# Performance work log

Hardware: AMD Instinct MI355X
Metric: run time of the kernel (lower is better)

Reference implementation:

```python
import jax, jax.numpy as jnp
import numpy as np

CDTYPE = jnp.complex64

# ---- 2x2 gate matrices (batched over events when theta is a vector) ----

def _rx(theta):
    h = theta * 0.5
    c = jnp.cos(h).astype(CDTYPE)
    s = (-1j) * jnp.sin(h).astype(CDTYPE)
    return jnp.stack([jnp.stack([c, s], -1), jnp.stack([s, c], -1)], -2)

def _ry(theta):
    h = theta * 0.5
    c = jnp.cos(h).astype(CDTYPE)
    s = jnp.sin(h).astype(CDTYPE)
    return jnp.stack([jnp.stack([c, -s], -1), jnp.stack([s, c], -1)], -2)

def _rz(theta):
    h = theta.astype(CDTYPE) * 0.5
    e0 = jnp.exp(-1j * h)
    e1 = jnp.exp(1j * h)
    z = jnp.zeros_like(e0)
    return jnp.stack([jnp.stack([e0, z], -1), jnp.stack([z, e1], -1)], -2)

# ---- batched statevector primitives (PennyLane convention: wire 0 = MSB) ----

def _apply(state, gate, wire):
    # state: (B, 2**n) complex; gate: (B,2,2) batched or (2,2) shared
    B = state.shape[0]
    st = state.reshape(B, 2 ** wire, 2, -1)
    if gate.ndim == 3:
        out = jnp.einsum('bij,bajc->baic', gate, st)
    else:
        out = jnp.einsum('ij,bajc->baic', gate, st)
    return out.reshape(B, -1)

def _cnot(state, c, t, n):
    # flip target axis on the control=1 half (pure permutation)
    B = state.shape[0]
    s = state.reshape((B,) + (2,) * n)
    i0 = [slice(None)] * (n + 1); i0[c + 1] = slice(0, 1)
    i1 = [slice(None)] * (n + 1); i1[c + 1] = slice(1, 2)
    s1 = jnp.flip(s[tuple(i1)], axis=t + 1)
    return jnp.concatenate([s[tuple(i0)], s1], axis=c + 1).reshape(B, -1)

def _expz(state, w):
    B = state.shape[0]
    p = (state.real ** 2 + state.imag ** 2).reshape(B, 2 ** w, 2, -1)
    return jnp.sum(p[:, :, 0, :], axis=(1, 2)) - jnp.sum(p[:, :, 1, :], axis=(1, 2))

def _qae_block(pt, eta, phi, weights, n, latent, trash, depth):
    B = pt.shape[0]
    state = jnp.zeros((B, 2 ** n), CDTYPE).at[:, 0].set(1.0)
    # angle encoding: RX(eta) RY(pt) RZ(phi) per wire (RX(0)=I covers MET)
    for k in range(n):
        state = _apply(state, _rx(eta[:, k]), k)
        state = _apply(state, _ry(pt[:, k]), k)
        state = _apply(state, _rz(phi[:, k]), k)
    for d in range(depth):
        for t in trash:
            for l in latent:
                state = _cnot(state, t, l, n)
        for k in range(n):
            state = _apply(state, _ry(weights[d * n + k]), k)  # shared (2,2) gate
        for l in latent:
            for t in trash:
                state = _cnot(state, l, t, n)
    return jnp.stack([_expz(state, w) for w in trash], axis=1)

def _forward(x, met_w, ele_w, mu_w, jet_w):
    B = x.shape[0]
    z = jnp.zeros((B, 1), x.dtype)
    met = _qae_block(x[:, 0:1], z, x[:, 1:2], met_w, 1, [], [0], 1)
    ele = _qae_block(x[:, 2:6], x[:, 6:10], x[:, 10:14], ele_w, 4, [0, 1], [2, 3], 1)
    mu = _qae_block(x[:, 14:18], x[:, 18:22], x[:, 22:26], mu_w, 4, [0, 1], [2, 3], 1)
    jet = _qae_block(x[:, 26:36], x[:, 36:46], x[:, 46:56], jet_w, 10,
                     [0, 1, 2, 3, 4, 5], [6, 7, 8, 9], 4)
    return met, ele, mu, jet

def setup_inputs() -> dict:
    key = jax.random.key(0)
    k0, k1, k2, k3, k4 = jax.random.split(key, 5)
    B = 4096
    return {
        'x': jax.random.normal(k0, (B, 56), dtype=jnp.float32),
        'met_weights': 0.01 * jax.random.normal(k1, (1,), dtype=jnp.float32),
        'ele_weights': 0.01 * jax.random.normal(k2, (4,), dtype=jnp.float32),
        'mu_weights': 0.01 * jax.random.normal(k3, (4,), dtype=jnp.float32),
        'jet_weights': 0.01 * jax.random.normal(k4, (40,), dtype=jnp.float32),
    }

def reference(x, met_weights, ele_weights, mu_weights, jet_weights):
    # returns (met (B,1), ele (B,2), mu (B,2), jet (B,4)) trash-wire Z expectations
    return _forward(x, met_weights, ele_weights, mu_weights, jet_weights)
```

## Files before the change

### kernel.cpp

```cpp
#include <hip/hip_runtime.h>
#include <hip/hip_bf16.h>


struct cplx { float re, im; };

__device__ __forceinline__ cplx cmul(cplx a, cplx b) {
  cplx r; r.re = a.re*b.re - a.im*b.im; r.im = a.re*b.im + a.im*b.re; return r;
}
__device__ __forceinline__ cplx csel(int c, cplx a, cplx b) {
  cplx r; r.re = c ? a.re : b.re; r.im = c ? a.im : b.im; return r;
}
__device__ __forceinline__ cplx shflx(cplx v, int m) {
  cplx r; r.re = __shfl_xor(v.re, m, 64); r.im = __shfl_xor(v.im, m, 64); return r;
}

__device__ __forceinline__ void enc_col(float pt, float eta, float phi,
                                        cplx* A, cplx* Bq) {
  float cx = __cosf(0.5f*eta), sx = __sinf(0.5f*eta);
  float cy = __cosf(0.5f*pt),  sy = __sinf(0.5f*pt);
  float cz = __cosf(0.5f*phi), sz = __sinf(0.5f*phi);
  float u = cy*cx, v = sy*sx;
  float p = sy*cx, q = -cy*sx;
  A->re  = cz*u + sz*v;  A->im  = cz*v - sz*u;
  Bq->re = cz*p - sz*q;  Bq->im = cz*q + sz*p;
}

__device__ void jet_sim(const float* __restrict__ xr, const float* __restrict__ jw,
                        float* __restrict__ out, int b, int lane, int jet_off) {
  cplx A[10], Bw[10];
  #pragma unroll
  for (int k = 0; k < 10; ++k)
    enc_col(xr[26+k], xr[36+k], xr[46+k], &A[k], &Bw[k]);

  cplx lf = csel((lane >> 5) & 1, Bw[4], A[4]);
  #pragma unroll
  for (int k = 5; k < 10; ++k)
    lf = cmul(lf, csel((lane >> (9-k)) & 1, Bw[k], A[k]));

  cplx st[16];
  #pragma unroll
  for (int r = 0; r < 16; ++r) {
    cplx f = lf;
    #pragma unroll
    for (int k = 0; k < 4; ++k)
      f = cmul(f, csel((r >> (3-k)) & 1, Bw[k], A[k]));
    st[r] = f;
  }

  const int p1 = __popc(lane & 15) & 1;
  const int lp = __popc(lane >> 4) & 1;

  for (int d = 0; d < 4; ++d) {
    #pragma unroll
    for (int r = 0; r < 8; ++r) {
      cplx v1 = st[r], v2 = st[r^15];
      cplx o1 = shflx(v2, 48);
      cplx o2 = shflx(v1, 48);
      st[r]    = csel(p1, o1, v1);
      st[r^15] = csel(p1, o2, v2);
    }
    float c[10], s[10];
    #pragma unroll
    for (int k = 0; k < 10; ++k) {
      float a = 0.5f * jw[d*10 + k];
      c[k] = __cosf(a); s[k] = __sinf(a);
    }
    #pragma unroll
    for (int k = 0; k < 4; ++k) {
      const int mr = 1 << (3-k);
      #pragma unroll
      for (int r = 0; r < 16; ++r) {
        if (!(r & mr)) {
          cplx a = st[r], bb = st[r|mr];
          st[r].re    = c[k]*a.re - s[k]*bb.re;
          st[r].im    = c[k]*a.im - s[k]*bb.im;
          st[r|mr].re = s[k]*a.re + c[k]*bb.re;
          st[r|mr].im = s[k]*a.im + c[k]*bb.im;
        }
      }
    }
    #pragma unroll
    for (int k = 4; k < 10; ++k) {
      const int lm = 1 << (9-k);
      const float sg = (lane & lm) ? s[k] : -s[k];
      #pragma unroll
      for (int r = 0; r < 16; ++r) {
        cplx o = shflx(st[r], lm);
        st[r].re = c[k]*st[r].re + sg*o.re;
        st[r].im = c[k]*st[r].im + sg*o.im;
      }
    }
    #pragma unroll
    for (int r = 0; r < 16; ++r) {
      cplx o = shflx(st[r], 15);
      const int p2 = (lp ^ (__popc(r) & 1)) & 1;
      st[r] = csel(p2, o, st[r]);
    }
  }

  float pr = 0.f;
  #pragma unroll
  for (int r = 0; r < 16; ++r)
    pr += st[r].re*st[r].re + st[r].im*st[r].im;
  pr += __shfl_xor(pr, 16, 64);
  pr += __shfl_xor(pr, 32, 64);
  float y = pr;
  #pragma unroll
  for (int j = 1; j <= 8; j <<= 1) {
    float aa = __shfl_xor(y, j, 64);
    y = (lane & j) ? (aa - y) : (y + aa);
  }
  if (lane == 8) out[jet_off + b*4 + 0] = y;
  if (lane == 4) out[jet_off + b*4 + 1] = y;
  if (lane == 2) out[jet_off + b*4 + 2] = y;
  if (lane == 1) out[jet_off + b*4 + 3] = y;
}

__device__ void sim4(const float* __restrict__ pt, const float* __restrict__ eta,
                     const float* __restrict__ phi, const float* __restrict__ w,
                     float* z_w2, float* z_w3) {
  cplx A[4], Bw[4];
  #pragma unroll
  for (int k = 0; k < 4; ++k)
    enc_col(pt[k], eta[k], phi[k], &A[k], &Bw[k]);

  cplx st[16];
  #pragma unroll
  for (int i = 0; i < 16; ++i) {
    cplx f = csel((i>>3)&1, Bw[0], A[0]);
    f = cmul(f, csel((i>>2)&1, Bw[1], A[1]));
    f = cmul(f, csel((i>>1)&1, Bw[2], A[2]));
    f = cmul(f, csel( i    &1, Bw[3], A[3]));
    st[i] = f;
  }
  cplx t;
  t = st[1]; st[1] = st[13]; st[13] = t;
  t = st[2]; st[2] = st[14]; st[14] = t;
  t = st[5]; st[5] = st[9];  st[9]  = t;
  t = st[6]; st[6] = st[10]; st[10] = t;
  #pragma unroll
  for (int k = 0; k < 4; ++k) {
    float a5 = 0.5f * w[k];
    float c = __cosf(a5), s = __sinf(a5);
    const int m = 8 >> k;
    #pragma unroll
    for (int i = 0; i < 16; ++i) {
      if (!(i & m)) {
        cplx a = st[i], bb = st[i|m];
        st[i].re   = c*a.re - s*bb.re;  st[i].im   = c*a.im - s*bb.im;
        st[i|m].re = s*a.re + c*bb.re;  st[i|m].im = s*a.im + c*bb.im;
      }
    }
  }
  t = st[4]; st[4] = st[7];  st[7]  = t;
  t = st[5]; st[5] = st[6];  st[6]  = t;
  t = st[8]; st[8] = st[11]; st[11] = t;
  t = st[9]; st[9] = st[10]; st[10] = t;

  float z2 = 0.f, z3 = 0.f;
  #pragma unroll
  for (int i = 0; i < 16; ++i) {
    float p = st[i].re*st[i].re + st[i].im*st[i].im;
    z2 += ((i>>1)&1) ? -p : p;
    z3 += ( i    &1) ? -p : p;
  }
  *z_w2 = z2; *z_w3 = z3;
}

__global__ __launch_bounds__(256)
void qae_kernel(const float* __restrict__ x,
                const float* __restrict__ met_w,
                const float* __restrict__ ele_w,
                const float* __restrict__ mu_w,
                const float* __restrict__ jet_w,
                float* __restrict__ out, int B, int jet_blocks) {
  if ((int)blockIdx.x < jet_blocks) {
    int wave = blockIdx.x * 4 + (threadIdx.x >> 6);
    int lane = threadIdx.x & 63;
    if (wave < B)
      jet_sim(x + (size_t)wave*56, jet_w, out, wave, lane, 5*B);
  } else {
    int b = (blockIdx.x - jet_blocks) * 256 + threadIdx.x;
    if (b >= B) return;
    const float* xr = x + (size_t)b*56;
    {
      float pt = xr[0], phi = xr[1], mw = met_w[0];
      float cy = __cosf(0.5f*pt),  sy = __sinf(0.5f*pt);
      float cz = __cosf(0.5f*phi), sz = __sinf(0.5f*phi);
      float cw = __cosf(0.5f*mw),  sw = __sinf(0.5f*mw);
      cplx al; al.re = cz*cy; al.im = -sz*cy;
      cplx be; be.re = cz*sy; be.im =  sz*sy;
      cplx a0; a0.re = cw*al.re - sw*be.re; a0.im = cw*al.im - sw*be.im;
      cplx a1; a1.re = sw*al.re + cw*be.re; a1.im = sw*al.im + cw*be.im;
      out[b] = (a0.re*a0.re + a0.im*a0.im) - (a1.re*a1.re + a1.im*a1.im);
    }
    float z2, z3;
    sim4(xr+2,  xr+6,  xr+10, ele_w, &z2, &z3);
    out[B   + b*2 + 0] = z2;  out[B   + b*2 + 1] = z3;
    sim4(xr+14, xr+18, xr+22, mu_w, &z2, &z3);
    out[3*B + b*2 + 0] = z2;  out[3*B + b*2 + 1] = z3;
  }
}

extern "C" void kernel_launch(void* const* d_in, const int* in_sizes, int n_in,
                              void* d_out, int out_size, void* d_ws, size_t ws_size,
                              hipStream_t stream) {
  const float* x     = (const float*)d_in[0];
  const float* met_w = (const float*)d_in[1];
  const float* ele_w = (const float*)d_in[2];
  const float* mu_w  = (const float*)d_in[3];
  const float* jet_w = (const float*)d_in[4];
  float* out = (float*)d_out;
  int B = in_sizes[0] / 56;
  int jet_blocks   = (B * 64 + 255) / 256;
  int small_blocks = (B + 255) / 256;
  qae_kernel<<<dim3(jet_blocks + small_blocks), dim3(256), 0, stream>>>(
      x, met_w, ele_w, mu_w, jet_w, out, B, jet_blocks);
}
```

Measured before the change: 106.0 us.

## Split each jet event's statevector across two waves with LDS exchange

Each jet event now runs on a 128-thread block, two waves, instead of one wave. Each lane holds 8 amplitudes instead of 16, and one qubit (wire 6) is mapped to the wave index. That qubit's gate and CNOT mixing are done through a shared-memory exchange with the partner wave, using block barriers. The aim is to halve per-thread register state and raise parallelism and occupancy, at the cost of LDS traffic, __syncthreads per depth layer, and a final cross-wave reduction.

```diff
diff --git a/kernel.cpp b/kernel.cpp
--- a/kernel.cpp
+++ b/kernel.cpp
@@ -25,97 +25,6 @@
   Bq->re = cz*p - sz*q;  Bq->im = cz*q + sz*p;
 }
 
-__device__ void jet_sim(const float* __restrict__ xr, const float* __restrict__ jw,
-                        float* __restrict__ out, int b, int lane, int jet_off) {
-  cplx A[10], Bw[10];
-  #pragma unroll
-  for (int k = 0; k < 10; ++k)
-    enc_col(xr[26+k], xr[36+k], xr[46+k], &A[k], &Bw[k]);
-
-  cplx lf = csel((lane >> 5) & 1, Bw[4], A[4]);
-  #pragma unroll
-  for (int k = 5; k < 10; ++k)
-    lf = cmul(lf, csel((lane >> (9-k)) & 1, Bw[k], A[k]));
-
-  cplx st[16];
-  #pragma unroll
-  for (int r = 0; r < 16; ++r) {
-    cplx f = lf;
-    #pragma unroll
-    for (int k = 0; k < 4; ++k)
-      f = cmul(f, csel((r >> (3-k)) & 1, Bw[k], A[k]));
-    st[r] = f;
-  }
-
-  const int p1 = __popc(lane & 15) & 1;
-  const int lp = __popc(lane >> 4) & 1;
-
-  for (int d = 0; d < 4; ++d) {
-    #pragma unroll
-    for (int r = 0; r < 8; ++r) {
-      cplx v1 = st[r], v2 = st[r^15];
-      cplx o1 = shflx(v2, 48);
-      cplx o2 = shflx(v1, 48);
-      st[r]    = csel(p1, o1, v1);
-      st[r^15] = csel(p1, o2, v2);
-    }
-    float c[10], s[10];
-    #pragma unroll
-    for (int k = 0; k < 10; ++k) {
-      float a = 0.5f * jw[d*10 + k];
-      c[k] = __cosf(a); s[k] = __sinf(a);
-    }
-    #pragma unroll
-    for (int k = 0; k < 4; ++k) {
-      const int mr = 1 << (3-k);
-      #pragma unroll
-      for (int r = 0; r < 16; ++r) {
-        if (!(r & mr)) {
-          cplx a = st[r], bb = st[r|mr];
-          st[r].re    = c[k]*a.re - s[k]*bb.re;
-          st[r].im    = c[k]*a.im - s[k]*bb.im;
-          st[r|mr].re = s[k]*a.re + c[k]*bb.re;
-          st[r|mr].im = s[k]*a.im + c[k]*bb.im;
-        }
-      }
-    }
-    #pragma unroll
-    for (int k = 4; k < 10; ++k) {
-      const int lm = 1 << (9-k);
-      const float sg = (lane & lm) ? s[k] : -s[k];
-      #pragma unroll
-      for (int r = 0; r < 16; ++r) {
-        cplx o = shflx(st[r], lm);
-        st[r].re = c[k]*st[r].re + sg*o.re;
-        st[r].im = c[k]*st[r].im + sg*o.im;
-      }
-    }
-    #pragma unroll
-    for (int r = 0; r < 16; ++r) {
-      cplx o = shflx(st[r], 15);
-      const int p2 = (lp ^ (__popc(r) & 1)) & 1;
-      st[r] = csel(p2, o, st[r]);
-    }
-  }
-
-  float pr = 0.f;
-  #pragma unroll
-  for (int r = 0; r < 16; ++r)
-    pr += st[r].re*st[r].re + st[r].im*st[r].im;
-  pr += __shfl_xor(pr, 16, 64);
-  pr += __shfl_xor(pr, 32, 64);
-  float y = pr;
-  #pragma unroll
-  for (int j = 1; j <= 8; j <<= 1) {
-    float aa = __shfl_xor(y, j, 64);
-    y = (lane & j) ? (aa - y) : (y + aa);
-  }
-  if (lane == 8) out[jet_off + b*4 + 0] = y;
-  if (lane == 4) out[jet_off + b*4 + 1] = y;
-  if (lane == 2) out[jet_off + b*4 + 2] = y;
-  if (lane == 1) out[jet_off + b*4 + 3] = y;
-}
-
 __device__ void sim4(const float* __restrict__ pt, const float* __restrict__ eta,
                      const float* __restrict__ phi, const float* __restrict__ w,
                      float* z_w2, float* z_w3) {
@@ -167,20 +76,135 @@
   *z_w2 = z2; *z_w3 = z3;
 }
 
-__global__ __launch_bounds__(256)
+__global__ __launch_bounds__(128)
 void qae_kernel(const float* __restrict__ x,
                 const float* __restrict__ met_w,
                 const float* __restrict__ ele_w,
                 const float* __restrict__ mu_w,
                 const float* __restrict__ jet_w,
-                float* __restrict__ out, int B, int jet_blocks) {
-  if ((int)blockIdx.x < jet_blocks) {
-    int wave = blockIdx.x * 4 + (threadIdx.x >> 6);
-    int lane = threadIdx.x & 63;
-    if (wave < B)
-      jet_sim(x + (size_t)wave*56, jet_w, out, wave, lane, 5*B);
+                float* __restrict__ out, int B) {
+  __shared__ float sm[128*18 + 16];
+  if ((int)blockIdx.x < B) {
+    const int b    = blockIdx.x;
+    const int tid  = threadIdx.x;
+    const int lane = tid & 63;
+    const int w    = tid >> 6;
+    const float* xr = x + (size_t)b*56;
+
+    cplx A[10], Bw[10];
+    #pragma unroll
+    for (int k = 0; k < 10; ++k)
+      enc_col(xr[26+k], xr[36+k], xr[46+k], &A[k], &Bw[k]);
+
+    cplx lf = csel((lane>>5)&1, Bw[3], A[3]);
+    lf = cmul(lf, csel((lane>>4)&1, Bw[4], A[4]));
+    lf = cmul(lf, csel((lane>>3)&1, Bw[5], A[5]));
+    lf = cmul(lf, csel(w,           Bw[6], A[6]));
+    lf = cmul(lf, csel((lane>>2)&1, Bw[7], A[7]));
+    lf = cmul(lf, csel((lane>>1)&1, Bw[8], A[8]));
+    lf = cmul(lf, csel( lane    &1, Bw[9], A[9]));
+
+    cplx st[8];
+    #pragma unroll
+    for (int r = 0; r < 8; ++r) {
+      cplx f = cmul(lf, csel((r>>2)&1, Bw[0], A[0]));
+      f = cmul(f, csel((r>>1)&1, Bw[1], A[1]));
+      f = cmul(f, csel( r    &1, Bw[2], A[2]));
+      st[r] = f;
+    }
+
+    const int pt_par  = (__popc(lane & 7) + w) & 1;
+    const int pl_lane = __popc((lane>>3) & 7) & 1;
+    float2* myb = (float2*)(sm + tid*18);
+    float2* pb  = (float2*)(sm + (tid^64)*18);
+
+    #pragma unroll
+    for (int d = 0; d < 4; ++d) {
+      #pragma unroll
+      for (int r = 0; r < 4; ++r) {
+        cplx v1 = st[r], v2 = st[r^7];
+        cplx o1 = shflx(v2, 0x38), o2 = shflx(v1, 0x38);
+        st[r]   = csel(pt_par, o1, v1);
+        st[r^7] = csel(pt_par, o2, v2);
+      }
+      float c[10], s[10];
+      #pragma unroll
+      for (int k = 0; k < 10; ++k) {
+        float a = 0.5f * jet_w[d*10 + k];
+        c[k] = __cosf(a); s[k] = __sinf(a);
+      }
+      #pragma unroll
+      for (int k = 0; k < 3; ++k) {
+        const int mr = 4 >> k;
+        #pragma unroll
+        for (int r = 0; r < 8; ++r) {
+          if (!(r & mr)) {
+            cplx a = st[r], bb = st[r|mr];
+            st[r].re    = c[k]*a.re - s[k]*bb.re;
+            st[r].im    = c[k]*a.im - s[k]*bb.im;
+            st[r|mr].re = s[k]*a.re + c[k]*bb.re;
+            st[r|mr].im = s[k]*a.im + c[k]*bb.im;
+          }
+        }
+      }
+      #pragma unroll
+      for (int kk = 0; kk < 6; ++kk) {
+        const int k  = (kk < 3) ? (3 + kk) : (4 + kk);
+        const int lm = (kk < 3) ? (32 >> kk) : (4 >> (kk-3));
+        const float sg = (lane & lm) ? s[k] : -s[k];
+        #pragma unroll
+        for (int r = 0; r < 8; ++r) {
+          cplx o = shflx(st[r], lm);
+          st[r].re = c[k]*st[r].re + sg*o.re;
+          st[r].im = c[k]*st[r].im + sg*o.im;
+        }
+      }
+      #pragma unroll
+      for (int r = 0; r < 8; ++r) myb[r] = make_float2(st[r].re, st[r].im);
+      __syncthreads();
+      cplx q[8];
+      #pragma unroll
+      for (int r = 0; r < 8; ++r) { float2 v = pb[r]; q[r].re = v.x; q[r].im = v.y; }
+      __syncthreads();
+      const float sg6 = w ? s[6] : -s[6];
+      #pragma unroll
+      for (int r = 0; r < 8; ++r) {
+        cplx keep;
+        keep.re = c[6]*st[r].re + sg6*q[r].re;
+        keep.im = c[6]*st[r].im + sg6*q[r].im;
+        cplx qs = shflx(q[r], 7), ss = shflx(st[r], 7);
+        cplx mov;
+        mov.re = c[6]*qs.re - sg6*ss.re;
+        mov.im = c[6]*qs.im - sg6*ss.im;
+        const int pl = (pl_lane + __popc(r)) & 1;
+        st[r] = csel(pl, mov, keep);
+      }
+    }
+
+    float pr = 0.f;
+    #pragma unroll
+    for (int r = 0; r < 8; ++r) pr += st[r].re*st[r].re + st[r].im*st[r].im;
+    pr += __shfl_xor(pr, 8, 64);
+    pr += __shfl_xor(pr, 16, 64);
+    pr += __shfl_xor(pr, 32, 64);
+    float y = pr;
+    #pragma unroll
+    for (int j = 1; j <= 4; j <<= 1) {
+      float aa = __shfl_xor(y, j, 64);
+      y = (lane & j) ? (aa - y) : (y + aa);
+    }
+    float* red = sm + 128*18;
+    if (lane < 8) red[w*8 + lane] = y;
+    __syncthreads();
+    if (tid == 0) {
+      float* o = out + (size_t)5*B + (size_t)b*4;
+      o[0] = red[0] - red[8];
+      o[1] = red[4] + red[12];
+      o[2] = red[2] + red[10];
+      o[3] = red[1] + red[9];
+    }
   } else {
-    int b = (blockIdx.x - jet_blocks) * 256 + threadIdx.x;
+    int b = ((int)blockIdx.x - B) * 128 + threadIdx.x;
     if (b >= B) return;
     const float* xr = x + (size_t)b*56;
     {
@@ -212,8 +236,8 @@
   const float* jet_w = (const float*)d_in[4];
   float* out = (float*)d_out;
   int B = in_sizes[0] / 56;
-  int jet_blocks   = (B * 64 + 255) / 256;
-  int small_blocks = (B + 255) / 256;
-  qae_kernel<<<dim3(jet_blocks + small_blocks), dim3(256), 0, stream>>>(
-      x, met_w, ele_w, mu_w, jet_w, out, B, jet_blocks);
-}
+  int jet_blocks   = B;
+  int small_blocks = (B + 127) / 128;
+  qae_kernel<<<dim3(jet_blocks + small_blocks), dim3(128), 0, stream>>>(
+      x, met_w, ele_w, mu_w, jet_w, out, B);
+}
```

After: 119.6 us. 12.8% more time.

## Remap jet statevector so lane bits hold wires 0-5 and use DPP shuffles

Applied to the files above, without the earlier changes.

Reassigns the 10-qubit jet state layout so the six lane bits hold wires 0-5 and the per-thread register index holds wires 6-9. This turns the CNOT permutation into a single bpermute on odd-parity registers plus an in-register swap. Lane-crossing RY rotations now use DPP and ds_swizzle instead of generic shuffles where possible, and trig uses sincos. The final reduction becomes a full butterfly over four accumulators. Launch bounds add a minimum-occupancy hint, and the jet block count is computed directly.

```diff
diff --git a/kernel.cpp b/kernel.cpp
--- a/kernel.cpp
+++ b/kernel.cpp
@@ -10,8 +10,24 @@
 __device__ __forceinline__ cplx csel(int c, cplx a, cplx b) {
   cplx r; r.re = c ? a.re : b.re; r.im = c ? a.im : b.im; return r;
 }
-__device__ __forceinline__ cplx shflx(cplx v, int m) {
-  cplx r; r.re = __shfl_xor(v.re, m, 64); r.im = __shfl_xor(v.im, m, 64); return r;
+
+template<int CTRL, int ROW, int BANK, bool BC>
+__device__ __forceinline__ float dppf(float oldv, float v) {
+  return __int_as_float(__builtin_amdgcn_update_dpp(
+      __float_as_int(oldv), __float_as_int(v), CTRL, ROW, BANK, BC));
+}
+__device__ __forceinline__ float xor1f(float v) { return dppf<0xB1, 0xF, 0xF, true>(v, v); }
+__device__ __forceinline__ float xor2f(float v) { return dppf<0x4E, 0xF, 0xF, true>(v, v); }
+__device__ __forceinline__ float xor8f(float v) { return dppf<0x128, 0xF, 0xF, true>(v, v); }
+__device__ __forceinline__ float xor4f(float v) {
+  float t = dppf<0x104, 0xF, 0xA, false>(v, v);
+  return    dppf<0x114, 0xF, 0x5, false>(t, v);
+}
+__device__ __forceinline__ float xor16f(float v) {
+  return __int_as_float(__builtin_amdgcn_ds_swizzle(__float_as_int(v), 0x401F));
+}
+__device__ __forceinline__ float bpermf(int addr, float v) {
+  return __int_as_float(__builtin_amdgcn_ds_bpermute(addr, __float_as_int(v)));
 }
 
 __device__ __forceinline__ void enc_col(float pt, float eta, float phi,
@@ -26,48 +42,72 @@
 }
 
 __device__ void jet_sim(const float* __restrict__ xr, const float* __restrict__ jw,
-                        float* __restrict__ out, int b, int lane, int jet_off) {
+                        float* __restrict__ out, int b, int lane, int B) {
   cplx A[10], Bw[10];
   #pragma unroll
   for (int k = 0; k < 10; ++k)
     enc_col(xr[26+k], xr[36+k], xr[46+k], &A[k], &Bw[k]);
 
-  cplx lf = csel((lane >> 5) & 1, Bw[4], A[4]);
-  #pragma unroll
-  for (int k = 5; k < 10; ++k)
-    lf = cmul(lf, csel((lane >> (9-k)) & 1, Bw[k], A[k]));
+  cplx f = csel((lane>>5)&1, Bw[0], A[0]);
+  f = cmul(f, csel((lane>>4)&1, Bw[1], A[1]));
+  f = cmul(f, csel((lane>>3)&1, Bw[2], A[2]));
+  f = cmul(f, csel((lane>>2)&1, Bw[3], A[3]));
+  f = cmul(f, csel((lane>>1)&1, Bw[4], A[4]));
+  f = cmul(f, csel( lane    &1, Bw[5], A[5]));
 
   cplx st[16];
-  #pragma unroll
-  for (int r = 0; r < 16; ++r) {
-    cplx f = lf;
-    #pragma unroll
-    for (int k = 0; k < 4; ++k)
-      f = cmul(f, csel((r >> (3-k)) & 1, Bw[k], A[k]));
-    st[r] = f;
-  }
-
-  const int p1 = __popc(lane & 15) & 1;
-  const int lp = __popc(lane >> 4) & 1;
-
+  {
+    cplx h6[2]; h6[0] = cmul(f, A[6]); h6[1] = cmul(f, Bw[6]);
+    cplx h7[4];
+    #pragma unroll
+    for (int j = 0; j < 2; ++j) { h7[2*j] = cmul(h6[j], A[7]); h7[2*j+1] = cmul(h6[j], Bw[7]); }
+    cplx h8[8];
+    #pragma unroll
+    for (int j = 0; j < 4; ++j) { h8[2*j] = cmul(h7[j], A[8]); h8[2*j+1] = cmul(h7[j], Bw[8]); }
+    #pragma unroll
+    for (int j = 0; j < 8; ++j) { st[2*j] = cmul(h8[j], A[9]); st[2*j+1] = cmul(h8[j], Bw[9]); }
+  }
+
+  const int a63 = (lane ^ 63) << 2;
+  const int a32 = (lane ^ 32) << 2;
+  const int pl  = __popc(lane) & 1;
+
+  #pragma unroll
   for (int d = 0; d < 4; ++d) {
-    #pragma unroll
-    for (int r = 0; r < 8; ++r) {
-      cplx v1 = st[r], v2 = st[r^15];
-      cplx o1 = shflx(v2, 48);
-      cplx o2 = shflx(v1, 48);
-      st[r]    = csel(p1, o1, v1);
-      st[r^15] = csel(p1, o2, v2);
-    }
     float c[10], s[10];
     #pragma unroll
-    for (int k = 0; k < 10; ++k) {
-      float a = 0.5f * jw[d*10 + k];
-      c[k] = __cosf(a); s[k] = __sinf(a);
-    }
-    #pragma unroll
-    for (int k = 0; k < 4; ++k) {
-      const int mr = 1 << (3-k);
+    for (int k = 0; k < 10; ++k) __sincosf(0.5f * jw[d*10 + k], &s[k], &c[k]);
+
+    #pragma unroll
+    for (int r = 0; r < 16; ++r) {
+      if (__popc(r) & 1) {
+        st[r].re = bpermf(a63, st[r].re);
+        st[r].im = bpermf(a63, st[r].im);
+      }
+    }
+
+#define LANE_RY(K, M, SHUF)                                   \
+    { const float cc = c[K];                                  \
+      const float sg = (lane & (M)) ? s[K] : -s[K];           \
+      _Pragma("unroll")                                       \
+      for (int r = 0; r < 16; ++r) {                          \
+        float ore = SHUF(st[r].re), oim = SHUF(st[r].im);     \
+        st[r].re = cc*st[r].re + sg*ore;                      \
+        st[r].im = cc*st[r].im + sg*oim;                      \
+      } }
+#define SH32(v) bpermf(a32, v)
+    LANE_RY(0, 32, SH32)
+    LANE_RY(1, 16, xor16f)
+    LANE_RY(2,  8, xor8f)
+    LANE_RY(3,  4, xor4f)
+    LANE_RY(4,  2, xor2f)
+    LANE_RY(5,  1, xor1f)
+#undef SH32
+#undef LANE_RY
+
+    #pragma unroll
+    for (int k = 6; k < 10; ++k) {
+      const int mr = 1 << (9-k);
       #pragma unroll
       for (int r = 0; r < 16; ++r) {
         if (!(r & mr)) {
@@ -79,41 +119,35 @@
         }
       }
     }
-    #pragma unroll
-    for (int k = 4; k < 10; ++k) {
-      const int lm = 1 << (9-k);
-      const float sg = (lane & lm) ? s[k] : -s[k];
-      #pragma unroll
-      for (int r = 0; r < 16; ++r) {
-        cplx o = shflx(st[r], lm);
-        st[r].re = c[k]*st[r].re + sg*o.re;
-        st[r].im = c[k]*st[r].im + sg*o.im;
-      }
-    }
-    #pragma unroll
-    for (int r = 0; r < 16; ++r) {
-      cplx o = shflx(st[r], 15);
-      const int p2 = (lp ^ (__popc(r) & 1)) & 1;
-      st[r] = csel(p2, o, st[r]);
-    }
-  }
-
-  float pr = 0.f;
-  #pragma unroll
-  for (int r = 0; r < 16; ++r)
-    pr += st[r].re*st[r].re + st[r].im*st[r].im;
-  pr += __shfl_xor(pr, 16, 64);
-  pr += __shfl_xor(pr, 32, 64);
-  float y = pr;
-  #pragma unroll
-  for (int j = 1; j <= 8; j <<= 1) {
-    float aa = __shfl_xor(y, j, 64);
-    y = (lane & j) ? (aa - y) : (y + aa);
-  }
-  if (lane == 8) out[jet_off + b*4 + 0] = y;
-  if (lane == 4) out[jet_off + b*4 + 1] = y;
-  if (lane == 2) out[jet_off + b*4 + 2] = y;
-  if (lane == 1) out[jet_off + b*4 + 3] = y;
+
+    #pragma unroll
+    for (int r = 0; r < 8; ++r) {
+      cplx a = st[r], bb = st[r^15];
+      st[r]    = csel(pl, bb, a);
+      st[r^15] = csel(pl, a, bb);
+    }
+  }
+
+  float z0 = 0.f, z1 = 0.f, z2 = 0.f, z3 = 0.f;
+  #pragma unroll
+  for (int r = 0; r < 16; ++r) {
+    float p = st[r].re*st[r].re + st[r].im*st[r].im;
+    z0 += (r & 8) ? -p : p;
+    z1 += (r & 4) ? -p : p;
+    z2 += (r & 2) ? -p : p;
+    z3 += (r & 1) ? -p : p;
+  }
+  #pragma unroll
+  for (int j = 1; j <= 32; j <<= 1) {
+    z0 += __shfl_xor(z0, j, 64);
+    z1 += __shfl_xor(z1, j, 64);
+    z2 += __shfl_xor(z2, j, 64);
+    z3 += __shfl_xor(z3, j, 64);
+  }
+  if (lane == 0) {
+    float* o = out + (size_t)5*B + (size_t)b*4;
+    o[0] = z0; o[1] = z1; o[2] = z2; o[3] = z3;
+  }
 }
 
 __device__ void sim4(const float* __restrict__ pt, const float* __restrict__ eta,
@@ -167,7 +201,7 @@
   *z_w2 = z2; *z_w3 = z3;
 }
 
-__global__ __launch_bounds__(256)
+__global__ __launch_bounds__(256, 4)
 void qae_kernel(const float* __restrict__ x,
                 const float* __restrict__ met_w,
                 const float* __restrict__ ele_w,
@@ -175,12 +209,12 @@
                 const float* __restrict__ jet_w,
                 float* __restrict__ out, int B, int jet_blocks) {
   if ((int)blockIdx.x < jet_blocks) {
-    int wave = blockIdx.x * 4 + (threadIdx.x >> 6);
+    int b = blockIdx.x * 4 + (threadIdx.x >> 6);
     int lane = threadIdx.x & 63;
-    if (wave < B)
-      jet_sim(x + (size_t)wave*56, jet_w, out, wave, lane, 5*B);
+    if (b < B)
+      jet_sim(x + (size_t)b*56, jet_w, out, b, lane, B);
   } else {
-    int b = (blockIdx.x - jet_blocks) * 256 + threadIdx.x;
+    int b = ((int)blockIdx.x - jet_blocks) * 256 + threadIdx.x;
     if (b >= B) return;
     const float* xr = x + (size_t)b*56;
     {
@@ -212,7 +246,7 @@
   const float* jet_w = (const float*)d_in[4];
   float* out = (float*)d_out;
   int B = in_sizes[0] / 56;
-  int jet_blocks   = (B * 64 + 255) / 256;
+  int jet_blocks   = (B + 3) / 4;
   int small_blocks = (B + 255) / 256;
   qae_kernel<<<dim3(jet_blocks + small_blocks), dim3(256), 0, stream>>>(
       x, met_w, ele_w, mu_w, jet_w, out, B, jet_blocks);
```

New measurement: 85.36 us. -19.5%, faster.
